# Kernel optimization log

Hardware: AMD Instinct MI355X
Metric: run time of the kernel (lower is better)

## Reference

```python
import jax, jax.numpy as jnp
import numpy as np

NUM_HEADS = 16
ROPE_BASE = 10000.0
LN_EPS = 1e-5


def _rope_tables(seq_len, head_dim, dtype):
    # half-dim angle table: (seq_len, head_dim//2)
    inv_freq = 1.0 / (ROPE_BASE ** (jnp.arange(0, head_dim, 2, dtype=jnp.float32) / head_dim))
    angles = jnp.arange(seq_len, dtype=jnp.float32)[:, None] * inv_freq[None, :]
    return jnp.cos(angles).astype(dtype), jnp.sin(angles).astype(dtype)


def _apply_rope(x, cos, sin):
    # x: (B, H, S, D_h); rotate interleaved (even, odd) dim pairs
    xe = x[..., 0::2]
    xo = x[..., 1::2]
    c = cos[None, None, :, :]
    s = sin[None, None, :, :]
    re = xe * c - xo * s
    ro = xe * s + xo * c
    return jnp.stack([re, ro], axis=-1).reshape(x.shape)


def _layernorm(x, g, b):
    mu = jnp.mean(x, axis=-1, keepdims=True)
    var = jnp.var(x, axis=-1, keepdims=True)
    return (x - mu) * jax.lax.rsqrt(var + LN_EPS) * g + b


def setup_inputs() -> dict:
    key = jax.random.key(0)
    ks = jax.random.split(key, 8)
    B, S, D, F = 2, 2048, 1024, 4096
    sd = lambda fan_in: 1.0 / np.sqrt(fan_in)
    return {
        "x": jax.random.normal(ks[0], (B, S, D), jnp.float32),
        "in_proj_w": jax.random.normal(ks[1], (3 * D, D), jnp.float32) * sd(D),
        "in_proj_b": jnp.zeros((3 * D,), jnp.float32),
        "out_w": jax.random.normal(ks[2], (D, D), jnp.float32) * sd(D),
        "out_b": jnp.zeros((D,), jnp.float32),
        "w1": jax.random.normal(ks[3], (F, D), jnp.float32) * sd(D),
        "b1": jnp.zeros((F,), jnp.float32),
        "w2": jax.random.normal(ks[4], (D, F), jnp.float32) * sd(F),
        "b2": jnp.zeros((D,), jnp.float32),
        "ln1_g": jnp.ones((D,), jnp.float32),
        "ln1_b": jnp.zeros((D,), jnp.float32),
        "ln2_g": jnp.ones((D,), jnp.float32),
        "ln2_b": jnp.zeros((D,), jnp.float32),
    }


def reference(x, in_proj_w, in_proj_b, out_w, out_b, w1, b1, w2, b2,
              ln1_g, ln1_b, ln2_g, ln2_b):
    B, S, D = x.shape
    H = NUM_HEADS
    Dh = D // H
    scale = Dh ** -0.5

    # fused QKV projection
    qkv = x @ in_proj_w.T + in_proj_b  # (B, S, 3D)
    q, k, v = jnp.split(qkv, 3, axis=-1)
    q = q.reshape(B, S, H, Dh).transpose(0, 2, 1, 3)
    k = k.reshape(B, S, H, Dh).transpose(0, 2, 1, 3)
    v = v.reshape(B, S, H, Dh).transpose(0, 2, 1, 3)

    cos, sin = _rope_tables(S, Dh, x.dtype)
    q = _apply_rope(q, cos, sin)
    k = _apply_rope(k, cos, sin)

    # SDPA (no mask, no dropout)
    scores = jnp.einsum('bhqd,bhkd->bhqk', q, k) * scale
    probs = jax.nn.softmax(scores, axis=-1)
    attn = jnp.einsum('bhqk,bhkd->bhqd', probs, v)
    attn = attn.transpose(0, 2, 1, 3).reshape(B, S, D)
    attn_out = attn @ out_w.T + out_b

    # post-norm encoder layer: residual + LN, FFN, residual + LN
    h = _layernorm(x + attn_out, ln1_g, ln1_b)
    ff = jax.nn.relu(h @ w1.T + b1) @ w2.T + b2
    return _layernorm(h + ff, ln2_g, ln2_b)
```

## Files before the change

kernel.cpp:

```cpp
#include <hip/hip_runtime.h>
#include <math.h>

typedef unsigned short u16;
typedef unsigned int u32;
typedef __attribute__((ext_vector_type(8))) __bf16 bf16x8;
typedef __attribute__((ext_vector_type(4))) float f32x4;

#define AS1 __attribute__((address_space(1)))
#define AS3 __attribute__((address_space(3)))

#define B_ 2
#define S_ 2048
#define D_ 1024
#define H_ 16
#define DH_ 64
#define F_ 4096
#define M_ 4096

__device__ __forceinline__ u16 f2b(float f) {
  u32 u = __builtin_bit_cast(u32, f);
  u += 0x7fffu + ((u >> 16) & 1u);
  return (u16)(u >> 16);
}

__device__ __forceinline__ u32 pack2(float a, float b) {
  u16 lo = __builtin_bit_cast(u16, (__bf16)a);
  u16 hi = __builtin_bit_cast(u16, (__bf16)b);
  return (u32)lo | ((u32)hi << 16);
}

__global__ __launch_bounds__(256) void cvt_kernel(const float* __restrict__ in,
                                                  u16* __restrict__ out, int n4) {
  int i = blockIdx.x * 256 + threadIdx.x;
  if (i < n4) {
    float4 v = ((const float4*)in)[i];
    ushort4 o;
    o.x = f2b(v.x); o.y = f2b(v.y); o.z = f2b(v.z); o.w = f2b(v.w);
    ((ushort4*)out)[i] = o;
  }
}

__global__ __launch_bounds__(256) void tables_kernel(float* __restrict__ cosT,
                                                     float* __restrict__ sinT) {
  int idx = blockIdx.x * 256 + threadIdx.x;
  int s = idx >> 5, i = idx & 31;
  float inv = powf(10000.0f, -(float)i / 32.0f);
  float ang = (float)s * inv;
  cosT[idx] = cosf(ang);
  sinT[idx] = sinf(ang);
}

template <bool BIAS, bool RELU, bool SPLIT, typename OutT>
__global__ __launch_bounds__(256) void gemm_bt(const u16* __restrict__ A,
                                               const u16* __restrict__ Bm,
                                               const float* __restrict__ bias,
                                               OutT* __restrict__ C, int M, int N, int K,
                                               int kChunk) {
  __shared__ u16 sA[128 * 32];
  __shared__ u16 sB[128 * 32];
  const int t = threadIdx.x;
  const int w = t >> 6, lane = t & 63;
  const int fr = lane & 15, fg = lane >> 4;
  const int row0 = blockIdx.y * 128, col0 = blockIdx.x * 128;
  const int wr = (w >> 1) * 64, wc = (w & 1) * 64;

  f32x4 acc[4][4] = {};

  const int rA = t >> 2;
  const int jj = ((t & 3) ^ ((t >> 3) & 3)) << 4;
  const int rdswz = ((fg ^ ((fr >> 1) & 3)) << 4);
  const char* aRead = (const char*)sA + (wr + fr) * 64 + rdswz;
  const char* bRead = (const char*)sB + (wc + fr) * 64 + rdswz;

  const int kb = blockIdx.z * kChunk;
  for (int k0 = kb; k0 < kb + kChunk; k0 += 32) {
#pragma unroll
    for (int i = 0; i < 2; ++i) {
      const char* srcA = (const char*)(A + (size_t)(row0 + i * 64 + rA) * K + k0) + jj;
      const char* srcB = (const char*)(Bm + (size_t)(col0 + i * 64 + rA) * K + k0) + jj;
      char* dA = (char*)sA + i * 4096 + w * 1024;
      char* dB = (char*)sB + i * 4096 + w * 1024;
      __builtin_amdgcn_global_load_lds((const AS1 u32*)srcA, (AS3 u32*)dA, 16, 0, 0);
      __builtin_amdgcn_global_load_lds((const AS1 u32*)srcB, (AS3 u32*)dB, 16, 0, 0);
    }
    __syncthreads();

    bf16x8 af[4], bfr[4];
#pragma unroll
    for (int m = 0; m < 4; ++m) af[m] = *(const bf16x8*)(aRead + m * 1024);
#pragma unroll
    for (int n = 0; n < 4; ++n) bfr[n] = *(const bf16x8*)(bRead + n * 1024);
#pragma unroll
    for (int m = 0; m < 4; ++m)
#pragma unroll
      for (int n = 0; n < 4; ++n)
        acc[m][n] = __builtin_amdgcn_mfma_f32_16x16x32_bf16(af[m], bfr[n], acc[m][n], 0, 0, 0);
    __syncthreads();
  }

  OutT* Cp = C;
  if constexpr (SPLIT) Cp = C + (size_t)blockIdx.z * M * N;
#pragma unroll
  for (int m = 0; m < 4; ++m) {
    const int rowb = row0 + wr + m * 16 + fg * 4;
#pragma unroll
    for (int n = 0; n < 4; ++n) {
      const int col = col0 + wc + n * 16 + fr;
      float bv = BIAS ? bias[col] : 0.0f;
      f32x4 c = acc[m][n];
#pragma unroll
      for (int r = 0; r < 4; ++r) {
        float v = c[r] + bv;
        if (RELU) v = fmaxf(v, 0.0f);
        if constexpr (sizeof(OutT) == 2)
          ((u16*)Cp)[(size_t)(rowb + r) * N + col] = f2b(v);
        else
          ((float*)Cp)[(size_t)(rowb + r) * N + col] = v;
      }
    }
  }
}

__global__ __launch_bounds__(256) void rope_kernel(const u16* __restrict__ qkv,
                                                   const float* __restrict__ cosT,
                                                   const float* __restrict__ sinT,
                                                   u16* __restrict__ qr, u16* __restrict__ kr,
                                                   u16* __restrict__ vt) {
  const int bh = blockIdx.x;
  const int b = bh >> 4, h = bh & 15;
  const int s0 = blockIdx.y * 64;
  const int t = threadIdx.x;

#pragma unroll
  for (int part = 0; part < 2; ++part) {
    const u16* src = qkv + (size_t)(b * S_ + s0) * (3 * D_) + part * D_ + h * DH_;
    u16* dst = (part ? kr : qr) + ((size_t)bh * S_ + s0) * DH_;
    const float psc = part ? 1.0f : 0.125f * 1.44269504088896340736f;
    for (int it = 0; it < 8; ++it) {
      int item = it * 256 + t;
      int sl = item >> 5, i = item & 31;
      u32 v = *(const u32*)(src + (size_t)sl * (3 * D_) + 2 * i);
      float xe = __builtin_bit_cast(float, v << 16);
      float xo = __builtin_bit_cast(float, v & 0xffff0000u);
      int s = s0 + sl;
      float c = cosT[s * 32 + i], sn = sinT[s * 32 + i];
      float re = (xe * c - xo * sn) * psc;
      float ro = (xe * sn + xo * c) * psc;
      *(u32*)(dst + (size_t)sl * DH_ + 2 * i) = pack2(re, ro);
    }
  }

  __shared__ u16 tile[64][65];
  const u16* vsrc = qkv + (size_t)(b * S_ + s0) * (3 * D_) + 2 * D_ + h * DH_;
  for (int it = 0; it < 16; ++it) {
    int sl = it * 4 + (t >> 6), dh = t & 63;
    tile[sl][dh] = vsrc[(size_t)sl * (3 * D_) + dh];
  }
  __syncthreads();
  u16* vdst = vt + (size_t)bh * DH_ * S_ + s0;
  for (int it = 0; it < 16; ++it) {
    int dh = it * 4 + (t >> 6), sl = t & 63;
    vdst[(size_t)dh * S_ + sl] = tile[sl][dh];
  }
}

__global__ __launch_bounds__(256) void attn_kernel(const u16* __restrict__ qr,
                                                   const u16* __restrict__ kr,
                                                   const u16* __restrict__ vt,
                                                   u16* __restrict__ attn) {
  __shared__ u16 sK[2][64 * 64];
  __shared__ u16 sV[2][64 * 64];
  __shared__ u16 plds[4][1024];
  const int bh = blockIdx.x;
  const int b = bh >> 4, h = bh & 15;
  const int q0 = blockIdx.y * 64;
  const int t = threadIdx.x, w = t >> 6, lane = t & 63;
  const int fr = lane & 15, fg = lane >> 4;

  const int qrow = q0 + w * 16 + fr;
  const u16* qbase = qr + ((size_t)bh * S_ + qrow) * DH_;
  bf16x8 qf0 = *(const bf16x8*)(qbase + fg * 8);
  bf16x8 qf1 = *(const bf16x8*)(qbase + 32 + fg * 8);

  const char* kByte = (const char*)(kr + (size_t)bh * S_ * DH_);
  const char* vByte = (const char*)(vt + (size_t)bh * DH_ * S_);
  char* pbase = (char*)&plds[w][0];
  const int ci0 = w * 64 + lane;

  f32x4 oacc[4] = {};
  float psum_acc = 0.0f;
  const float M0 = 12.0f;

  auto stage = [&](int bufb, int kt) {
#pragma unroll
    for (int i = 0; i < 2; ++i) {
      int ci = i * 256 + ci0;
      int r = ci >> 3, j = ci & 7;
      int jj = j ^ (r & 7);
      const char* srcK = kByte + (size_t)(kt + r) * 128 + (jj << 4);
      const char* srcV = vByte + (size_t)r * (S_ * 2) + (size_t)kt * 2 + (jj << 4);
      char* dK = (char*)&sK[bufb][0] + i * 4096 + w * 1024;
      char* dV = (char*)&sV[bufb][0] + i * 4096 + w * 1024;
      __builtin_amdgcn_global_load_lds((const AS1 u32*)srcK, (AS3 u32*)dK, 16, 0, 0);
      __builtin_amdgcn_global_load_lds((const AS1 u32*)srcV, (AS3 u32*)dV, 16, 0, 0);
    }
  };

  stage(0, 0);
  __syncthreads();

  int buf = 0;
  for (int kt = 0; kt < S_; kt += 64) {
    if (kt + 64 < S_) stage(buf ^ 1, kt + 64);

    const char* kB = (const char*)&sK[buf][0];
    const char* vB = (const char*)&sV[buf][0];

    f32x4 st[4];
    __builtin_amdgcn_s_setprio(1);
#pragma unroll
    for (int ks = 0; ks < 4; ++ks) {
      const char* rowp = kB + (ks * 16 + fr) * 128;
      bf16x8 kf0 = *(const bf16x8*)(rowp + ((fg ^ (fr & 7)) << 4));
      bf16x8 kf1 = *(const bf16x8*)(rowp + (((fg + 4) ^ (fr & 7)) << 4));
      f32x4 z = {};
      z = __builtin_amdgcn_mfma_f32_16x16x32_bf16(kf0, qf0, z, 0, 0, 0);
      st[ks] = __builtin_amdgcn_mfma_f32_16x16x32_bf16(kf1, qf1, z, 0, 0, 0);
    }
    __builtin_amdgcn_s_setprio(0);

#pragma unroll
    for (int ks = 0; ks < 4; ++ks) {
      float p0 = __builtin_amdgcn_exp2f(st[ks][0] - M0);
      float p1 = __builtin_amdgcn_exp2f(st[ks][1] - M0);
      float p2 = __builtin_amdgcn_exp2f(st[ks][2] - M0);
      float p3 = __builtin_amdgcn_exp2f(st[ks][3] - M0);
      psum_acc += (p0 + p1) + (p2 + p3);
      int wb = fr * 128 + (((ks * 32) | (fg * 8)) ^ ((fr & 7) << 4));
      *(uint2*)(pbase + wb) = make_uint2(pack2(p0, p1), pack2(p2, p3));
    }

    asm volatile("s_waitcnt lgkmcnt(0)" ::: "memory");
    __builtin_amdgcn_sched_barrier(0);

    __builtin_amdgcn_s_setprio(1);
#pragma unroll
    for (int ksub = 0; ksub < 2; ++ksub) {
      int rb = fr * 128 + (((ksub * 64) | (fg * 16)) ^ ((fr & 7) << 4));
      bf16x8 pf = *(const bf16x8*)(pbase + rb);
#pragma unroll
      for (int d = 0; d < 4; ++d) {
        const char* vp = vB + (d * 16 + fr) * 128 + ((((ksub * 4) | fg) ^ (fr & 7)) << 4);
        bf16x8 vf = *(const bf16x8*)vp;
        oacc[d] = __builtin_amdgcn_mfma_f32_16x16x32_bf16(vf, pf, oacc[d], 0, 0, 0);
      }
    }
    __builtin_amdgcn_s_setprio(0);
    __syncthreads();
    buf ^= 1;
  }

  psum_acc += __shfl_xor(psum_acc, 16);
  psum_acc += __shfl_xor(psum_acc, 32);
  const float inv_l = 1.0f / psum_acc;
  u16* obase = attn + (size_t)(b * S_ + q0 + w * 16 + fr) * D_ + h * DH_;
#pragma unroll
  for (int d = 0; d < 4; ++d) {
    ushort4 o4;
    o4.x = f2b(oacc[d][0] * inv_l);
    o4.y = f2b(oacc[d][1] * inv_l);
    o4.z = f2b(oacc[d][2] * inv_l);
    o4.w = f2b(oacc[d][3] * inv_l);
    *(ushort4*)(obase + d * 16 + fg * 4) = o4;
  }
}

template <int NS, bool WRITE_BF16>
__global__ __launch_bounds__(256) void reduce_ln_kernel(const float* __restrict__ parts,
                                                        const float* __restrict__ bias,
                                                        const float* __restrict__ resid,
                                                        const float* __restrict__ gamma,
                                                        const float* __restrict__ beta,
                                                        float* __restrict__ outf,
                                                        u16* __restrict__ outb) {
  const int row = blockIdx.x;
  const int t = threadIdx.x;
  const size_t base = (size_t)row * D_;
  float4 v = ((const float4*)bias)[t];
  {
    const float4 r4 = ((const float4*)(resid + base))[t];
    v.x += r4.x; v.y += r4.y; v.z += r4.z; v.w += r4.w;
  }
#pragma unroll
  for (int s = 0; s < NS; ++s) {
    const float4 p4 = ((const float4*)(parts + (size_t)s * M_ * D_ + base))[t];
    v.x += p4.x; v.y += p4.y; v.z += p4.z; v.w += p4.w;
  }
  float s = v.x + v.y + v.z + v.w;
  float ss = v.x * v.x + v.y * v.y + v.z * v.z + v.w * v.w;
#pragma unroll
  for (int off = 1; off < 64; off <<= 1) {
    s += __shfl_xor(s, off);
    ss += __shfl_xor(ss, off);
  }
  __shared__ float red[8];
  const int w = t >> 6, lane = t & 63;
  if (lane == 0) { red[w] = s; red[4 + w] = ss; }
  __syncthreads();
  s = red[0] + red[1] + red[2] + red[3];
  ss = red[4] + red[5] + red[6] + red[7];
  const float mu = s * (1.0f / D_);
  const float var = ss * (1.0f / D_) - mu * mu;
  const float rstd = rsqrtf(var + 1e-5f);
  const float4 g4 = ((const float4*)gamma)[t];
  const float4 b4 = ((const float4*)beta)[t];
  float4 o;
  o.x = (v.x - mu) * rstd * g4.x + b4.x;
  o.y = (v.y - mu) * rstd * g4.y + b4.y;
  o.z = (v.z - mu) * rstd * g4.z + b4.z;
  o.w = (v.w - mu) * rstd * g4.w + b4.w;
  ((float4*)(outf + base))[t] = o;
  if constexpr (WRITE_BF16) {
    ushort4 ob;
    ob.x = f2b(o.x); ob.y = f2b(o.y); ob.z = f2b(o.z); ob.w = f2b(o.w);
    ((ushort4*)(outb + base))[t] = ob;
  }
}

extern "C" void kernel_launch(void* const* d_in, const int* in_sizes, int n_in,
                              void* d_out, int out_size, void* d_ws, size_t ws_size,
                              hipStream_t stream) {
  const float* x = (const float*)d_in[0];
  const float* in_proj_w = (const float*)d_in[1];
  const float* in_proj_b = (const float*)d_in[2];
  const float* out_w = (const float*)d_in[3];
  const float* out_b = (const float*)d_in[4];
  const float* w1 = (const float*)d_in[5];
  const float* b1 = (const float*)d_in[6];
  const float* w2 = (const float*)d_in[7];
  const float* b2 = (const float*)d_in[8];
  const float* ln1_g = (const float*)d_in[9];
  const float* ln1_b = (const float*)d_in[10];
  const float* ln2_g = (const float*)d_in[11];
  const float* ln2_b = (const float*)d_in[12];

  char* ws = (char*)d_ws;
  u16* wib = (u16*)(ws + 0);
  u16* wob = (u16*)(ws + 6291456);
  u16* w1b = (u16*)(ws + 8388608);
  u16* w2b = (u16*)(ws + 16777216);
  float* cosT = (float*)(ws + 25165824);
  float* sinT = (float*)(ws + 25427968);
  u16* qkvb = (u16*)(ws + 25690112);
  float* part = (float*)(ws + 25690112);
  u16* qrb = (u16*)(ws + 59244544);
  u16* krb = (u16*)(ws + 67633152);
  u16* vtb = (u16*)(ws + 76021760);
  u16* attnb = (u16*)(ws + 84410368);
  u16* ff = (u16*)(ws + 59244544);
  u16* xb = (u16*)(ws + 92798976);
  float* hf = (float*)(ws + 92798976);
  u16* hb = (u16*)(ws + 109576192);
  (void)ws_size; (void)in_sizes; (void)n_in; (void)out_size;

  cvt_kernel<<<4096, 256, 0, stream>>>(x, xb, 1048576);
  cvt_kernel<<<3072, 256, 0, stream>>>(in_proj_w, wib, 786432);
  cvt_kernel<<<1024, 256, 0, stream>>>(out_w, wob, 262144);
  cvt_kernel<<<4096, 256, 0, stream>>>(w1, w1b, 1048576);
  cvt_kernel<<<4096, 256, 0, stream>>>(w2, w2b, 1048576);
  tables_kernel<<<256, 256, 0, stream>>>(cosT, sinT);

  gemm_bt<true, false, false, u16><<<dim3(24, 32), 256, 0, stream>>>(
      xb, wib, in_proj_b, qkvb, M_, 3 * D_, D_, D_);

  rope_kernel<<<dim3(32, 32), 256, 0, stream>>>(qkvb, cosT, sinT, qrb, krb, vtb);

  attn_kernel<<<dim3(32, 32), 256, 0, stream>>>(qrb, krb, vtb, attnb);

  gemm_bt<false, false, true, float><<<dim3(8, 32, 2), 256, 0, stream>>>(
      attnb, wob, nullptr, part, M_, D_, D_, 512);
  reduce_ln_kernel<2, true><<<4096, 256, 0, stream>>>(part, out_b, x, ln1_g, ln1_b, hf, hb);

  gemm_bt<true, true, false, u16><<<dim3(32, 32), 256, 0, stream>>>(
      hb, w1b, b1, ff, M_, F_, D_, D_);

  gemm_bt<false, false, true, float><<<dim3(8, 32, 2), 256, 0, stream>>>(
      ff, w2b, nullptr, part, M_, D_, F_, 2048);
  reduce_ln_kernel<2, false><<<4096, 256, 0, stream>>>(part, b2, hf, ln2_g, ln2_b,
                                                       (float*)d_out, nullptr);
}
```

Baseline: 394.7 us.

## Store split-K partials as bf16, merge conversion kernels, raise FFN2 split to four

The split-K partial sums from the output-projection and FFN2 GEMMs are now written as bf16 instead of fp32, which halves the partial-buffer traffic in both the GEMM epilogue and the reduce+LayerNorm kernel. The five fp32-to-bf16 conversion launches are merged into one kernel that selects its source and destination by index range, removing launch overhead. FFN2 now splits K four ways instead of two, giving more blocks for parallelism in exchange for more partial reads. Rounding the partials to bf16 before the residual and LayerNorm adds precision error.

```diff
diff --git a/kernel.cpp b/kernel.cpp
--- a/kernel.cpp
+++ b/kernel.cpp
@@ -23,21 +23,33 @@
   return (u16)(u >> 16);
 }
 
+__device__ __forceinline__ float b2f(u16 b) {
+  return __builtin_bit_cast(float, (u32)b << 16);
+}
+
 __device__ __forceinline__ u32 pack2(float a, float b) {
   u16 lo = __builtin_bit_cast(u16, (__bf16)a);
   u16 hi = __builtin_bit_cast(u16, (__bf16)b);
   return (u32)lo | ((u32)hi << 16);
 }
 
-__global__ __launch_bounds__(256) void cvt_kernel(const float* __restrict__ in,
-                                                  u16* __restrict__ out, int n4) {
+__global__ __launch_bounds__(256) void cvt5_kernel(const float* __restrict__ s0, u16* __restrict__ d0,
+                                                   const float* __restrict__ s1, u16* __restrict__ d1,
+                                                   const float* __restrict__ s2, u16* __restrict__ d2,
+                                                   const float* __restrict__ s3, u16* __restrict__ d3,
+                                                   const float* __restrict__ s4, u16* __restrict__ d4) {
   int i = blockIdx.x * 256 + threadIdx.x;
-  if (i < n4) {
-    float4 v = ((const float4*)in)[i];
-    ushort4 o;
-    o.x = f2b(v.x); o.y = f2b(v.y); o.z = f2b(v.z); o.w = f2b(v.w);
-    ((ushort4*)out)[i] = o;
-  }
+  const float* src;
+  u16* dst;
+  if (i < 1048576) { src = s0; dst = d0; }
+  else if (i < 1835008) { src = s1; dst = d1; i -= 1048576; }
+  else if (i < 2097152) { src = s2; dst = d2; i -= 1835008; }
+  else if (i < 3145728) { src = s3; dst = d3; i -= 2097152; }
+  else { src = s4; dst = d4; i -= 3145728; }
+  float4 v = ((const float4*)src)[i];
+  ushort4 o;
+  o.x = f2b(v.x); o.y = f2b(v.y); o.z = f2b(v.z); o.w = f2b(v.w);
+  ((ushort4*)dst)[i] = o;
 }
 
 __global__ __launch_bounds__(256) void tables_kernel(float* __restrict__ cosT,
@@ -276,7 +288,7 @@
 }
 
 template <int NS, bool WRITE_BF16>
-__global__ __launch_bounds__(256) void reduce_ln_kernel(const float* __restrict__ parts,
+__global__ __launch_bounds__(256) void reduce_ln_kernel(const u16* __restrict__ parts,
                                                         const float* __restrict__ bias,
                                                         const float* __restrict__ resid,
                                                         const float* __restrict__ gamma,
@@ -293,8 +305,8 @@
   }
 #pragma unroll
   for (int s = 0; s < NS; ++s) {
-    const float4 p4 = ((const float4*)(parts + (size_t)s * M_ * D_ + base))[t];
-    v.x += p4.x; v.y += p4.y; v.z += p4.z; v.w += p4.w;
+    const ushort4 p4 = ((const ushort4*)(parts + (size_t)s * M_ * D_ + base))[t];
+    v.x += b2f(p4.x); v.y += b2f(p4.y); v.z += b2f(p4.z); v.w += b2f(p4.w);
   }
   float s = v.x + v.y + v.z + v.w;
   float ss = v.x * v.x + v.y * v.y + v.z * v.z + v.w * v.w;
@@ -352,7 +364,7 @@
   float* cosT = (float*)(ws + 25165824);
   float* sinT = (float*)(ws + 25427968);
   u16* qkvb = (u16*)(ws + 25690112);
-  float* part = (float*)(ws + 25690112);
+  u16* partb = (u16*)(ws + 25690112);
   u16* qrb = (u16*)(ws + 59244544);
   u16* krb = (u16*)(ws + 67633152);
   u16* vtb = (u16*)(ws + 76021760);
@@ -363,11 +375,7 @@
   u16* hb = (u16*)(ws + 109576192);
   (void)ws_size; (void)in_sizes; (void)n_in; (void)out_size;
 
-  cvt_kernel<<<4096, 256, 0, stream>>>(x, xb, 1048576);
-  cvt_kernel<<<3072, 256, 0, stream>>>(in_proj_w, wib, 786432);
-  cvt_kernel<<<1024, 256, 0, stream>>>(out_w, wob, 262144);
-  cvt_kernel<<<4096, 256, 0, stream>>>(w1, w1b, 1048576);
-  cvt_kernel<<<4096, 256, 0, stream>>>(w2, w2b, 1048576);
+  cvt5_kernel<<<16384, 256, 0, stream>>>(x, xb, in_proj_w, wib, out_w, wob, w1, w1b, w2, w2b);
   tables_kernel<<<256, 256, 0, stream>>>(cosT, sinT);
 
   gemm_bt<true, false, false, u16><<<dim3(24, 32), 256, 0, stream>>>(
@@ -377,15 +385,15 @@
 
   attn_kernel<<<dim3(32, 32), 256, 0, stream>>>(qrb, krb, vtb, attnb);
 
-  gemm_bt<false, false, true, float><<<dim3(8, 32, 2), 256, 0, stream>>>(
-      attnb, wob, nullptr, part, M_, D_, D_, 512);
-  reduce_ln_kernel<2, true><<<4096, 256, 0, stream>>>(part, out_b, x, ln1_g, ln1_b, hf, hb);
+  gemm_bt<false, false, true, u16><<<dim3(8, 32, 2), 256, 0, stream>>>(
+      attnb, wob, nullptr, partb, M_, D_, D_, 512);
+  reduce_ln_kernel<2, true><<<4096, 256, 0, stream>>>(partb, out_b, x, ln1_g, ln1_b, hf, hb);
 
   gemm_bt<true, true, false, u16><<<dim3(32, 32), 256, 0, stream>>>(
       hb, w1b, b1, ff, M_, F_, D_, D_);
 
-  gemm_bt<false, false, true, float><<<dim3(8, 32, 2), 256, 0, stream>>>(
-      ff, w2b, nullptr, part, M_, D_, F_, 2048);
-  reduce_ln_kernel<2, false><<<4096, 256, 0, stream>>>(part, b2, hf, ln2_g, ln2_b,
+  gemm_bt<false, false, true, u16><<<dim3(8, 32, 4), 256, 0, stream>>>(
+      ff, w2b, nullptr, partb, M_, D_, F_, 1024);
+  reduce_ln_kernel<4, false><<<4096, 256, 0, stream>>>(partb, b2, hf, ln2_g, ln2_b,
                                                        (float*)d_out, nullptr);
 }
```

Measured after the change: 394.5 us. No clear change (-0.0%).
